# Kernel optimization log

Hardware: AMD Instinct MI355X
Metric: run time of the kernel (lower is better)

The kernel has to match this reference:

```python
import jax, jax.numpy as jnp
import numpy as np

EPS = 1e-12  # torch F.normalize eps


def _l1_normalize(x, axis):
    denom = jnp.maximum(jnp.sum(jnp.abs(x), axis=axis, keepdims=True), EPS)
    return x / denom


def setup_inputs() -> dict:
    key = jax.random.key(0)
    k1, k2, k3, k4, k5 = jax.random.split(key, 5)
    B, N, M, F_atom, F_bond, F_out = 16, 1024, 12, 128, 32, 128
    stdv = 1.0 / np.sqrt(F_out)
    atom = jax.random.normal(k1, (B, N, F_atom), dtype=jnp.float32)
    bond = jax.random.normal(k2, (B, N, M, F_bond), dtype=jnp.float32)
    adj_matrix = jax.random.randint(k3, (B, N, M), 0, N, dtype=jnp.int64)
    weight_atom_1 = jax.random.uniform(k4, (F_atom, F_out), dtype=jnp.float32, minval=-stdv, maxval=stdv)
    bias_atom_1 = jax.random.uniform(k5, (F_out,), dtype=jnp.float32, minval=-stdv, maxval=stdv)
    return {
        "atom": atom,
        "bond": bond,
        "adj_matrix": adj_matrix,
        "weight_atom_1": weight_atom_1,
        "bias_atom_1": bias_atom_1,
    }


def reference(atom, bond, adj_matrix, weight_atom_1, bias_atom_1):
    # atom: (B,N,F); bond: (B,N,M,Fb); adj_matrix: (B,N,M)
    # Per-batch neighbor gather: atom_neighbor[b,n,m] = atom[b, adj[b,n,m]]
    atom_neighbor = jax.vmap(lambda a, idx: a[idx])(atom, adj_matrix)  # (B,N,M,F)
    atom_neighbor = jnp.mean(atom_neighbor, axis=-2)  # (B,N,F)

    # Bond-norm chain
    bond_norm = jnp.sqrt(jnp.sum(bond * bond, axis=-1))       # (B,N,M) L2 norm
    bond_norm = bond_norm ** (-2.0)                            # inverse square
    bond_norm = _l1_normalize(bond_norm, axis=-1)              # over M
    bond_norm = jnp.prod(bond_norm, axis=2)                    # (B,N)
    bond_norm = _l1_normalize(bond_norm, axis=0)               # over B
    bond_norm = bond_norm ** (-1.0)
    bond_norm = _l1_normalize(bond_norm, axis=1)               # over N

    atom_update = (atom + atom_neighbor) * bond_norm[:, :, None]
    atom_update = jnp.matmul(atom_update, weight_atom_1) + bias_atom_1
    return jax.nn.relu(atom_update)
```

## Files before the change

### kernel.cpp

```cpp
#include <hip/hip_runtime.h>
#include <hip/hip_bf16.h>

#define EPS 1e-12f

typedef __bf16 bf16x8 __attribute__((ext_vector_type(8)));
typedef __bf16 bf16x4 __attribute__((ext_vector_type(4)));
typedef float  f32x4  __attribute__((ext_vector_type(4)));


__global__ __launch_bounds__(256) void k_bond(const float* __restrict__ bond,
                                              const float* __restrict__ W,
                                              float* __restrict__ p_out,
                                              __bf16* __restrict__ Wt) {
    const int t = threadIdx.x;
    if (blockIdx.x < 256) {
        const int gtid = blockIdx.x * 256 + t;
        const int row  = gtid >> 2;
        const int q    = gtid & 3;
        const float* base = bond + (size_t)row * 384 + q * 96;

        float x[3];
#pragma unroll
        for (int mm = 0; mm < 3; ++mm) {
            float s = 0.f;
#pragma unroll
            for (int j = 0; j < 8; ++j) {
                f32x4 v = __builtin_nontemporal_load((const f32x4*)(base + mm * 32 + j * 4));
                s = fmaf(v.x, v.x, s);
                s = fmaf(v.y, v.y, s);
                s = fmaf(v.z, v.z, s);
                s = fmaf(v.w, v.w, s);
            }
            x[mm] = 1.0f / s;
        }
        float sum  = x[0] + x[1] + x[2];
        float prod = x[0] * x[1] * x[2];
        sum  += __shfl_xor(sum, 1);  prod *= __shfl_xor(prod, 1);
        sum  += __shfl_xor(sum, 2);  prod *= __shfl_xor(prod, 2);
        if (q == 0) {
            float d   = fmaxf(sum, EPS);
            float d2  = d * d, d3 = d2 * d, d6 = d3 * d3;
            p_out[row] = prod / (d6 * d6);
        }
    } else {
        const int base = (blockIdx.x - 256) * 4096;
#pragma unroll
        for (int i = 0; i < 16; ++i) {
            int idx = base + t + 256 * i;
            int k = idx >> 7, j = idx & 127;
            Wt[j * 128 + k] = (__bf16)W[idx];
        }
    }
}

__global__ __launch_bounds__(256) void k_main(const float* __restrict__ atom,
                                              const int* __restrict__ adj,
                                              const float* __restrict__ p,
                                              const __bf16* __restrict__ Wt,
                                              const float* __restrict__ bias,
                                              float* __restrict__ out) {
    __shared__ __bf16 uA[64][136];
    __shared__ float  sScale[64] __attribute__((aligned(16)));
    __shared__ int    sAdj[64 * 12];
    __shared__ float  red[4];

    const int t = threadIdx.x;
    const int blk = blockIdx.x;
    const int b   = (blk & 7) | (((blk >> 7) & 1) << 3);
    const int nlo = ((blk >> 3) & 15) * 64;
    const int rowbase = b * 1024 + nlo;

    for (int idx = t; idx < 64 * 12; idx += 256) sAdj[idx] = adj[rowbase * 12 + idx];

    const int n0 = t * 4;
    f32x4 cs = {0.f, 0.f, 0.f, 0.f};
#pragma unroll
    for (int bb = 0; bb < 16; ++bb) cs += *(const f32x4*)(p + bb * 1024 + n0);
    f32x4 pb = *(const f32x4*)(p + b * 1024 + n0);
    f32x4 r4;
    r4.x = fmaxf(cs.x, EPS) / pb.x;
    r4.y = fmaxf(cs.y, EPS) / pb.y;
    r4.z = fmaxf(cs.z, EPS) / pb.z;
    r4.w = fmaxf(cs.w, EPS) / pb.w;
    float S_part = r4.x + r4.y + r4.z + r4.w;
#pragma unroll
    for (int off = 32; off >= 1; off >>= 1) S_part += __shfl_xor(S_part, off);
    if ((t & 63) == 0) red[t >> 6] = S_part;
    __syncthreads();
    const float invS = 1.0f / fmaxf(red[0] + red[1] + red[2] + red[3], EPS);
    if (n0 >= nlo && n0 < nlo + 64) *(f32x4*)&sScale[n0 - nlo] = r4 * invS;
    __syncthreads();

    {
        const int jc = (t & 31) * 4;
        const int rg = t >> 5;
        const float* atomB = atom + (size_t)b * (1024 * 128);
#pragma unroll
        for (int i = 0; i < 8; ++i) {
            const int r = rg + i * 8;
            f32x4 a = {0.f, 0.f, 0.f, 0.f};
#pragma unroll
            for (int m = 0; m < 12; ++m) {
                int idx = sAdj[r * 12 + m];
                a += *(const f32x4*)(atomB + (size_t)idx * 128 + jc);
            }
            f32x4 own = *(const f32x4*)(atomB + (size_t)(nlo + r) * 128 + jc);
            f32x4 u = (own + a * (1.0f / 12.0f)) * sScale[r];
            bf16x4 ub;
            ub.x = (__bf16)u.x; ub.y = (__bf16)u.y; ub.z = (__bf16)u.z; ub.w = (__bf16)u.w;
            *(bf16x4*)&uA[r][jc] = ub;
        }
    }
    __syncthreads();

    const int wave = t >> 6, lane = t & 63;
    const int r0 = wave * 16;
    const int quad = lane >> 4, lrow = lane & 15;

    bf16x8 aF[4];
#pragma unroll
    for (int kc = 0; kc < 4; ++kc)
        aF[kc] = *(const bf16x8*)&uA[r0 + lrow][kc * 32 + quad * 8];

    f32x4 acc[8];
#pragma unroll
    for (int nt = 0; nt < 8; ++nt) acc[nt] = (f32x4){0.f, 0.f, 0.f, 0.f};

#pragma unroll
    for (int nt = 0; nt < 8; ++nt) {
        const int col = nt * 16 + lrow;
        const __bf16* wb = Wt + col * 128 + quad * 8;
#pragma unroll
        for (int kc = 0; kc < 4; ++kc) {
            bf16x8 bF = *(const bf16x8*)(wb + kc * 32);
            acc[nt] = __builtin_amdgcn_mfma_f32_16x16x32_bf16(aF[kc], bF, acc[nt], 0, 0, 0);
        }
    }

#pragma unroll
    for (int nt = 0; nt < 8; ++nt) {
        const int col = nt * 16 + lrow;
        const float bv = bias[col];
#pragma unroll
        for (int i = 0; i < 4; ++i) {
            const int r = r0 + quad * 4 + i;
            float v = fmaxf(acc[nt][i] + bv, 0.f);
            __builtin_nontemporal_store(v, &out[(size_t)(rowbase + r) * 128 + col]);
        }
    }
}

extern "C" void kernel_launch(void* const* d_in, const int* in_sizes, int n_in,
                              void* d_out, int out_size, void* d_ws, size_t ws_size,
                              hipStream_t stream) {
    const float* atom = (const float*)d_in[0];
    const float* bond = (const float*)d_in[1];
    const int*   adj  = (const int*)d_in[2];
    const float* W    = (const float*)d_in[3];
    const float* bias = (const float*)d_in[4];
    float* out = (float*)d_out;

    char* ws = (char*)d_ws;
    float*  p  = (float*)ws;
    __bf16* Wt = (__bf16*)(ws + 65536);

    hipLaunchKernelGGL(k_bond, dim3(260), dim3(256), 0, stream, bond, W, p, Wt);
    hipLaunchKernelGGL(k_main, dim3(256), dim3(256), 0, stream, atom, adj, p, Wt, bias, out);
}
```

Baseline: 102.1 us.

## Fuse bond-norm and main kernels via global atomic grid barrier

Merges the bond-norm reduction kernel and the gather+MFMA kernel into one persistent launch of 256 blocks with 512 threads. Each block computes its own slice of bond norms and the W transpose, then all blocks meet at a global atomic-counter barrier before the cross-batch normalization. The aim is to drop one kernel launch and its gap and to double threads per block. The cost is an extra memset launch, and the barrier depends on all 256 blocks being resident at once, which risks deadlock if they are not.

```diff
diff --git a/kernel.cpp b/kernel.cpp
--- a/kernel.cpp
+++ b/kernel.cpp
@@ -8,87 +8,101 @@
 typedef float  f32x4  __attribute__((ext_vector_type(4)));
 
 
-__global__ __launch_bounds__(256) void k_bond(const float* __restrict__ bond,
-                                              const float* __restrict__ W,
-                                              float* __restrict__ p_out,
-                                              __bf16* __restrict__ Wt) {
-    const int t = threadIdx.x;
-    if (blockIdx.x < 256) {
-        const int gtid = blockIdx.x * 256 + t;
-        const int row  = gtid >> 2;
-        const int q    = gtid & 3;
-        const float* base = bond + (size_t)row * 384 + q * 96;
-
-        float x[3];
-#pragma unroll
-        for (int mm = 0; mm < 3; ++mm) {
-            float s = 0.f;
-#pragma unroll
-            for (int j = 0; j < 8; ++j) {
-                f32x4 v = __builtin_nontemporal_load((const f32x4*)(base + mm * 32 + j * 4));
-                s = fmaf(v.x, v.x, s);
-                s = fmaf(v.y, v.y, s);
-                s = fmaf(v.z, v.z, s);
-                s = fmaf(v.w, v.w, s);
-            }
-            x[mm] = 1.0f / s;
-        }
-        float sum  = x[0] + x[1] + x[2];
-        float prod = x[0] * x[1] * x[2];
-        sum  += __shfl_xor(sum, 1);  prod *= __shfl_xor(prod, 1);
-        sum  += __shfl_xor(sum, 2);  prod *= __shfl_xor(prod, 2);
-        if (q == 0) {
-            float d   = fmaxf(sum, EPS);
-            float d2  = d * d, d3 = d2 * d, d6 = d3 * d3;
-            p_out[row] = prod / (d6 * d6);
-        }
-    } else {
-        const int base = (blockIdx.x - 256) * 4096;
-#pragma unroll
-        for (int i = 0; i < 16; ++i) {
-            int idx = base + t + 256 * i;
-            int k = idx >> 7, j = idx & 127;
-            Wt[j * 128 + k] = (__bf16)W[idx];
-        }
-    }
-}
-
-__global__ __launch_bounds__(256) void k_main(const float* __restrict__ atom,
-                                              const int* __restrict__ adj,
-                                              const float* __restrict__ p,
-                                              const __bf16* __restrict__ Wt,
-                                              const float* __restrict__ bias,
-                                              float* __restrict__ out) {
+__global__ __launch_bounds__(512) void k_fused(const float* __restrict__ atom,
+                                               const float* __restrict__ bond,
+                                               const int* __restrict__ adj,
+                                               const float* __restrict__ W,
+                                               const float* __restrict__ bias,
+                                               float* __restrict__ out,
+                                               float* p, __bf16* Wt,
+                                               unsigned int* bar)
+{
     __shared__ __bf16 uA[64][136];
+    __shared__ float  xv[64][12];
     __shared__ float  sScale[64] __attribute__((aligned(16)));
     __shared__ int    sAdj[64 * 12];
     __shared__ float  red[4];
 
-    const int t = threadIdx.x;
-    const int blk = blockIdx.x;
+    const int t    = threadIdx.x;
+    const int blk  = blockIdx.x;
+    const int wave = t >> 6, lane = t & 63;
+
     const int b   = (blk & 7) | (((blk >> 7) & 1) << 3);
     const int nlo = ((blk >> 3) & 15) * 64;
     const int rowbase = b * 1024 + nlo;
 
-    for (int idx = t; idx < 64 * 12; idx += 256) sAdj[idx] = adj[rowbase * 12 + idx];
+    for (int idx = t; idx < 768; idx += 512) sAdj[idx] = adj[rowbase * 12 + idx];
 
-    const int n0 = t * 4;
-    f32x4 cs = {0.f, 0.f, 0.f, 0.f};
+    {
+        const float* wbase = bond + (size_t)(blk * 64 + wave * 8) * 384;
 #pragma unroll
-    for (int bb = 0; bb < 16; ++bb) cs += *(const f32x4*)(p + bb * 1024 + n0);
-    f32x4 pb = *(const f32x4*)(p + b * 1024 + n0);
-    f32x4 r4;
-    r4.x = fmaxf(cs.x, EPS) / pb.x;
-    r4.y = fmaxf(cs.y, EPS) / pb.y;
-    r4.z = fmaxf(cs.z, EPS) / pb.z;
-    r4.w = fmaxf(cs.w, EPS) / pb.w;
-    float S_part = r4.x + r4.y + r4.z + r4.w;
+        for (int i = 0; i < 12; ++i) {
+            f32x4 v = __builtin_nontemporal_load((const f32x4*)(wbase + (i * 64 + lane) * 4));
+            float s = v.x * v.x;
+            s = fmaf(v.y, v.y, s);
+            s = fmaf(v.z, v.z, s);
+            s = fmaf(v.w, v.w, s);
+            s += __shfl_xor(s, 1);
+            s += __shfl_xor(s, 2);
+            s += __shfl_xor(s, 4);
+            if ((lane & 7) == 0) {
+                const int g = i * 8 + (lane >> 3);
+                xv[wave * 8 + g / 12][g % 12] = s;
+            }
+        }
+    }
+
+    if (blk < 16) {
+        const int e = (blk * 512 + t) * 2;
+        const int k = e >> 7, j = e & 127;
+        float2 wv = *(const float2*)(W + e);
+        Wt[j * 128 + k]       = (__bf16)wv.x;
+        Wt[(j + 1) * 128 + k] = (__bf16)wv.y;
+    }
+    __syncthreads();
+
+    if (t < 64) {
+        float x[12], sum = 0.f, prod = 1.f;
 #pragma unroll
-    for (int off = 32; off >= 1; off >>= 1) S_part += __shfl_xor(S_part, off);
-    if ((t & 63) == 0) red[t >> 6] = S_part;
+        for (int m = 0; m < 12; ++m) x[m] = 1.0f / xv[t][m];
+#pragma unroll
+        for (int m = 0; m < 12; ++m) { sum += x[m]; prod *= x[m]; }
+        const float d = fmaxf(sum, EPS);
+        const float d2 = d * d, d3 = d2 * d, d6 = d3 * d3;
+        p[blk * 64 + t] = prod / (d6 * d6);
+    }
+
+    __threadfence();
     __syncthreads();
-    const float invS = 1.0f / fmaxf(red[0] + red[1] + red[2] + red[3], EPS);
-    if (n0 >= nlo && n0 < nlo + 64) *(f32x4*)&sScale[n0 - nlo] = r4 * invS;
+    if (t == 0) {
+        __hip_atomic_fetch_add(bar, 1u, __ATOMIC_RELEASE, __HIP_MEMORY_SCOPE_AGENT);
+        while (__hip_atomic_load(bar, __ATOMIC_RELAXED, __HIP_MEMORY_SCOPE_AGENT) < 256u)
+            __builtin_amdgcn_s_sleep(16);
+    }
+    __syncthreads();
+    __threadfence();
+
+    f32x4 r4 = {0.f, 0.f, 0.f, 0.f};
+    const int n0 = (t & 255) * 4;
+    if (t < 256) {
+        f32x4 cs = {0.f, 0.f, 0.f, 0.f};
+#pragma unroll
+        for (int bb = 0; bb < 16; ++bb) cs += *(const f32x4*)(p + bb * 1024 + n0);
+        f32x4 pb = *(const f32x4*)(p + b * 1024 + n0);
+        r4.x = fmaxf(cs.x, EPS) / pb.x;
+        r4.y = fmaxf(cs.y, EPS) / pb.y;
+        r4.z = fmaxf(cs.z, EPS) / pb.z;
+        r4.w = fmaxf(cs.w, EPS) / pb.w;
+        float S_part = r4.x + r4.y + r4.z + r4.w;
+#pragma unroll
+        for (int off = 32; off >= 1; off >>= 1) S_part += __shfl_xor(S_part, off);
+        if ((t & 63) == 0) red[t >> 6] = S_part;
+    }
+    __syncthreads();
+    if (t < 256) {
+        const float invS = 1.0f / fmaxf(red[0] + red[1] + red[2] + red[3], EPS);
+        if (n0 >= nlo && n0 < nlo + 64) *(f32x4*)&sScale[n0 - nlo] = r4 * invS;
+    }
     __syncthreads();
 
     {
@@ -96,8 +110,8 @@
         const int rg = t >> 5;
         const float* atomB = atom + (size_t)b * (1024 * 128);
 #pragma unroll
-        for (int i = 0; i < 8; ++i) {
-            const int r = rg + i * 8;
+        for (int i = 0; i < 4; ++i) {
+            const int r = rg + i * 16;
             f32x4 a = {0.f, 0.f, 0.f, 0.f};
 #pragma unroll
             for (int m = 0; m < 12; ++m) {
@@ -113,8 +127,8 @@
     }
     __syncthreads();
 
-    const int wave = t >> 6, lane = t & 63;
-    const int r0 = wave * 16;
+    const int wp = wave >> 1, half = wave & 1;
+    const int r0 = wp * 16;
     const int quad = lane >> 4, lrow = lane & 15;
 
     bf16x8 aF[4];
@@ -122,29 +136,29 @@
     for (int kc = 0; kc < 4; ++kc)
         aF[kc] = *(const bf16x8*)&uA[r0 + lrow][kc * 32 + quad * 8];
 
-    f32x4 acc[8];
+    f32x4 acc[4];
 #pragma unroll
-    for (int nt = 0; nt < 8; ++nt) acc[nt] = (f32x4){0.f, 0.f, 0.f, 0.f};
+    for (int q = 0; q < 4; ++q) acc[q] = (f32x4){0.f, 0.f, 0.f, 0.f};
 
 #pragma unroll
-    for (int nt = 0; nt < 8; ++nt) {
-        const int col = nt * 16 + lrow;
+    for (int q = 0; q < 4; ++q) {
+        const int col = (half * 4 + q) * 16 + lrow;
         const __bf16* wb = Wt + col * 128 + quad * 8;
 #pragma unroll
         for (int kc = 0; kc < 4; ++kc) {
             bf16x8 bF = *(const bf16x8*)(wb + kc * 32);
-            acc[nt] = __builtin_amdgcn_mfma_f32_16x16x32_bf16(aF[kc], bF, acc[nt], 0, 0, 0);
+            acc[q] = __builtin_amdgcn_mfma_f32_16x16x32_bf16(aF[kc], bF, acc[q], 0, 0, 0);
         }
     }
 
 #pragma unroll
-    for (int nt = 0; nt < 8; ++nt) {
-        const int col = nt * 16 + lrow;
+    for (int q = 0; q < 4; ++q) {
+        const int col = (half * 4 + q) * 16 + lrow;
         const float bv = bias[col];
 #pragma unroll
         for (int i = 0; i < 4; ++i) {
             const int r = r0 + quad * 4 + i;
-            float v = fmaxf(acc[nt][i] + bv, 0.f);
+            float v = fmaxf(acc[q][i] + bv, 0.f);
             __builtin_nontemporal_store(v, &out[(size_t)(rowbase + r) * 128 + col]);
         }
     }
@@ -163,7 +177,9 @@
     char* ws = (char*)d_ws;
     float*  p  = (float*)ws;
     __bf16* Wt = (__bf16*)(ws + 65536);
+    unsigned int* bar = (unsigned int*)(ws + 98304);
 
-    hipLaunchKernelGGL(k_bond, dim3(260), dim3(256), 0, stream, bond, W, p, Wt);
-    hipLaunchKernelGGL(k_main, dim3(256), dim3(256), 0, stream, atom, adj, p, Wt, bias, out);
+    hipMemsetAsync(bar, 0, 64, stream);
+    hipLaunchKernelGGL(k_fused, dim3(256), dim3(512), 0, stream,
+                       atom, bond, adj, W, bias, out, p, Wt, bar);
 }
```

After: 180.1 us. 76.5% more time.
